# Kernel optimization log

Hardware: AMD Instinct MI355X
Metric: run time of the kernel (lower is better)

The kernel has to match this reference:

```python
import jax, jax.numpy as jnp
import numpy as np

B = 4096      # batch
F = 26        # sparse fields
V = 100000    # vocab per field
D = 64        # emb_dim
A = 64        # att_vector
ND = 13       # dense features
FEA = ND + D  # 77, BN / DNN input width
HID = [FEA, 256, 128, 64]
EPS = 1e-5


def setup_inputs() -> dict:
    key = jax.random.key(0)
    ks = jax.random.split(key, 20)
    s = 0.05  # matches .normal_(0, 0.05) init
    inp = {
        "sx": jax.random.randint(ks[0], (B, F), 0, V),
        "dx": jax.random.normal(ks[1], (B, ND), dtype=jnp.float32),
        "emb_table": jax.random.normal(ks[2], (F, V, D), dtype=jnp.float32) * s,
        "att_w_W": jax.random.normal(ks[3], (D, A), dtype=jnp.float32) * s,
        "att_w_b": jnp.zeros((A,), jnp.float32),
        "att_d_W": jax.random.normal(ks[4], (A, 1), dtype=jnp.float32) * s,
        "att_d_b": jnp.zeros((1,), jnp.float32),
        "bn_gamma": jnp.ones((FEA,), jnp.float32),
        "bn_beta": jnp.zeros((FEA,), jnp.float32),
        "w1": jax.random.normal(ks[5], (HID[0], HID[1]), dtype=jnp.float32) * s,
        "b1": jnp.zeros((HID[1],), jnp.float32),
        "w2": jax.random.normal(ks[6], (HID[1], HID[2]), dtype=jnp.float32) * s,
        "b2": jnp.zeros((HID[2],), jnp.float32),
        "w3": jax.random.normal(ks[7], (HID[2], HID[3]), dtype=jnp.float32) * s,
        "b3": jnp.zeros((HID[3],), jnp.float32),
        "wf": jax.random.normal(ks[8], (HID[3], 1), dtype=jnp.float32) * s,
        "bf": jnp.zeros((1,), jnp.float32),
    }
    return inp


def _afm_forward(sx, dx, emb_table, att_w_W, att_w_b, att_d_W, att_d_b,
                 bn_gamma, bn_beta, w1, b1, w2, b2, w3, b3, wf, bf):
    # embedding gather: [B, F, D]
    embeds = emb_table[jnp.arange(F)[None, :], sx]
    # all pairwise field interactions (upper-triangular pairs)
    i1, i2 = np.triu_indices(F, k=1)          # P = F*(F-1)/2 = 325
    bi = embeds[:, i1, :] * embeds[:, i2, :]  # [B, P, D]
    # attention MLP + softmax-weighted sum pooling over pairs
    a = jax.nn.relu(jnp.einsum("bpd,da->bpa", bi, att_w_W) + att_w_b)
    scores = jnp.einsum("bpa,ao->bpo", a, att_d_W) + att_d_b  # [B, P, 1]
    w = jax.nn.softmax(scores, axis=1)
    att_out = jnp.sum(w * bi, axis=1)         # [B, D]
    # concat with dense, batchnorm (training-mode batch stats, biased var)
    x = jnp.concatenate([att_out, dx], axis=-1)  # [B, FEA]
    mu = jnp.mean(x, axis=0)
    var = jnp.mean((x - mu) ** 2, axis=0)
    x = (x - mu) * jax.lax.rsqrt(var + EPS) * bn_gamma + bn_beta
    # DNN tower (dropout=0.0 -> identity) + final linear + sigmoid
    x = jax.nn.relu(x @ w1 + b1)
    x = jax.nn.relu(x @ w2 + b2)
    x = jax.nn.relu(x @ w3 + b3)
    out = jax.nn.sigmoid(x @ wf + bf)
    return jnp.squeeze(out, axis=-1)          # [B]


def reference(sx, dx, emb_table, att_w_W, att_w_b, att_d_W, att_d_b,
              bn_gamma, bn_beta, w1, b1, w2, b2, w3, b3, wf, bf):
    return _afm_forward(sx, dx, emb_table, att_w_W, att_w_b, att_d_W, att_d_b,
                        bn_gamma, bn_beta, w1, b1, w2, b2, w3, b3, wf, bf)
```

## Files before the change

kernel.cpp:

```cpp
#include <hip/hip_runtime.h>
#include <hip/hip_bf16.h>
#include <math.h>

#define BSZ   4096
#define F     26
#define VOC   100000
#define D     64
#define AD    64
#define ND    13
#define FEA   77
#define NPAIR 325
#define NPAD  336
#define MT    21
#define EP    68
#define H1    256
#define H2    128
#define H3    64
#define EPSF  1e-5f
#define MROW  4

typedef __attribute__((ext_vector_type(8))) short short8;
typedef __attribute__((ext_vector_type(4))) float f32x4;

union FragU { short8 s; unsigned int u[4]; };

__device__ __forceinline__ unsigned int pk2bf(float a, float b) {
  __hip_bfloat162 h = __float22bfloat162_rn(make_float2(a, b));
  return *reinterpret_cast<unsigned int*>(&h);
}
__device__ __forceinline__ unsigned short f2bf(float f) {
  unsigned int u = __float_as_uint(f);
  u += 0x7fffu + ((u >> 16) & 1u);
  return (unsigned short)(u >> 16);
}
template<int CTRL>
__device__ __forceinline__ float dpp_add(float x) {
  int xi = __builtin_bit_cast(int, x);
  int yi = __builtin_amdgcn_update_dpp(xi, xi, CTRL, 0xf, 0xf, false);
  return x + __builtin_bit_cast(float, yi);
}
__device__ __forceinline__ float row16_sum(float x) {
  x = dpp_add<0xB1>(x);
  x = dpp_add<0x4E>(x);
  x = dpp_add<0x124>(x);
  x = dpp_add<0x128>(x);
  return x;
}
__device__ __forceinline__ float bcast_lane(float v, int l) {
  return __builtin_bit_cast(float,
      __builtin_amdgcn_readlane(__builtin_bit_cast(int, v), l));
}

__global__ __launch_bounds__(256, 4) void k_attn(
    const int* __restrict__ sx, const float* __restrict__ dx,
    const float* __restrict__ emb, const float* __restrict__ attW,
    const float* __restrict__ attb, const float* __restrict__ attdW,
    const float* __restrict__ attdb, float* __restrict__ x,
    float* __restrict__ partS, float* __restrict__ partQ)
{
  __shared__ __align__(16) float e_all[4][27 * EP];
  __shared__ __align__(16) float sc_all[4][NPAD];
  __shared__ float xblk[4][80];
  __shared__ unsigned short pt[NPAD];

  const int t    = threadIdx.x;
  const int lane = t & 63;
  const int wv   = t >> 6;
  const int b    = __builtin_amdgcn_readfirstlane(blockIdx.x * 4 + wv);

  for (int p = t; p < NPAD; p += 256) {
    int f1 = 26, f2 = 26;
    if (p < NPAIR) {
      int i = 0, rem = p;
      while (rem >= F - 1 - i) { rem -= F - 1 - i; ++i; }
      f1 = i; f2 = i + 1 + rem;
    }
    pt[p] = (unsigned short)(f1 | (f2 << 8));
  }

  float* e_w  = e_all[wv];
  float* sc_w = sc_all[wv];

  {
    const int* sxb = sx + b * F;
    int rows[F];
    #pragma unroll
    for (int f = 0; f < F; ++f) rows[f] = sxb[f];
    float vf[F];
    #pragma unroll
    for (int f = 0; f < F; ++f)
      vf[f] = emb[((size_t)f * VOC + rows[f]) * D + lane];
    #pragma unroll
    for (int f = 0; f < F; ++f) e_w[f * EP + lane] = vf[f];
    e_w[26 * EP + lane] = 0.f;
  }

  short8 bfrag[2][4];
  float bj[4], dwj[4];
  {
    const int kb = (lane >> 4) * 8;
    const int cl = lane & 15;
    #pragma unroll
    for (int kk = 0; kk < 2; ++kk)
      #pragma unroll
      for (int n = 0; n < 4; ++n)
        #pragma unroll
        for (int j = 0; j < 8; ++j) {
          int k = kk * 32 + kb + j;
          bfrag[kk][n][j] = (short)f2bf(attW[k * AD + n * 16 + cl]);
        }
    #pragma unroll
    for (int n = 0; n < 4; ++n) {
      bj[n]  = attb[n * 16 + cl];
      dwj[n] = attdW[n * 16 + cl];
    }
  }
  const float db0 = attdb[0];

  __syncthreads();

  const int row16 = lane & 15;
  const int kgrp  = lane >> 4;
  const int k0    = kgrp * 8;
  const f32x4 zero4 = {0.f, 0.f, 0.f, 0.f};
  #pragma unroll 2
  for (int m = 0; m < MT; ++m) {
    const int prow = m * 16 + row16;
    const unsigned short pp = pt[prow];
    const float* r1 = &e_w[(pp & 0xff) * EP];
    const float* r2 = &e_w[(pp >> 8) * EP];
    f32x4 xv0 = *(const f32x4*)&r1[k0];
    f32x4 xv1 = *(const f32x4*)&r1[k0 + 4];
    f32x4 yv0 = *(const f32x4*)&r2[k0];
    f32x4 yv1 = *(const f32x4*)&r2[k0 + 4];
    f32x4 xv2 = *(const f32x4*)&r1[32 + k0];
    f32x4 xv3 = *(const f32x4*)&r1[32 + k0 + 4];
    f32x4 yv2 = *(const f32x4*)&r2[32 + k0];
    f32x4 yv3 = *(const f32x4*)&r2[32 + k0 + 4];
    f32x4 pa = xv0 * yv0;
    f32x4 pb = xv1 * yv1;
    f32x4 pc = xv2 * yv2;
    f32x4 pd = xv3 * yv3;
    FragU a0, a1;
    a0.u[0] = pk2bf(pa[0], pa[1]); a0.u[1] = pk2bf(pa[2], pa[3]);
    a0.u[2] = pk2bf(pb[0], pb[1]); a0.u[3] = pk2bf(pb[2], pb[3]);
    a1.u[0] = pk2bf(pc[0], pc[1]); a1.u[1] = pk2bf(pc[2], pc[3]);
    a1.u[2] = pk2bf(pd[0], pd[1]); a1.u[3] = pk2bf(pd[2], pd[3]);

    f32x4 acc[4];
    #pragma unroll
    for (int n = 0; n < 4; ++n) {
      acc[n] = __builtin_amdgcn_mfma_f32_16x16x32_bf16(a0.s, bfrag[0][n], zero4, 0, 0, 0);
      acc[n] = __builtin_amdgcn_mfma_f32_16x16x32_bf16(a1.s, bfrag[1][n], acc[n], 0, 0, 0);
    }
    f32x4 vale = zero4;
    #pragma unroll
    for (int n = 0; n < 4; ++n) {
      f32x4 rl = __builtin_elementwise_max(acc[n] + bj[n], zero4);
      vale = rl * dwj[n] + vale;
    }
    float s0 = row16_sum(vale[0]) + db0;
    float s1 = row16_sum(vale[1]) + db0;
    float s2 = row16_sum(vale[2]) + db0;
    float s3 = row16_sum(vale[3]) + db0;
    if (row16 == 0) {
      float4 o = {s0, s1, s2, s3};
      *(float4*)&sc_w[m * 16 + kgrp * 4] = o;
    }
  }

  float sv[6], ev[6];
  float mx = -1e30f;
  #pragma unroll
  for (int i = 0; i < 6; ++i) {
    int idx = lane + 64 * i;
    sv[i] = (idx < NPAIR) ? sc_w[idx] : -1e30f;
    mx = fmaxf(mx, sv[i]);
  }
  #pragma unroll
  for (int off = 32; off; off >>= 1) mx = fmaxf(mx, __shfl_xor(mx, off));
  float s = 0.f;
  #pragma unroll
  for (int i = 0; i < 6; ++i) {
    int idx = lane + 64 * i;
    ev[i] = (idx < NPAIR) ? __expf(sv[i] - mx) : 0.f;
    s += ev[i];
  }
  #pragma unroll
  for (int off = 32; off; off >>= 1) s += __shfl_xor(s, off);
  const float invZ = 1.f / s;

  float ef[F];
  #pragma unroll
  for (int f = 0; f < F; ++f) ef[f] = e_w[f * EP + lane];

  float pa0 = 0.f, pa1 = 0.f, pa2 = 0.f, pa3 = 0.f;
  {
    int p = 0;
    #pragma unroll
    for (int f1 = 0; f1 < F - 1; ++f1) {
      #pragma unroll
      for (int f2 = f1 + 1; f2 < F; ++f2) {
        const float w = bcast_lane(ev[p >> 6], p & 63);
        const float prod = ef[f1] * ef[f2];
        if ((p & 3) == 0)      pa0 = fmaf(w, prod, pa0);
        else if ((p & 3) == 1) pa1 = fmaf(w, prod, pa1);
        else if ((p & 3) == 2) pa2 = fmaf(w, prod, pa2);
        else                   pa3 = fmaf(w, prod, pa3);
        ++p;
      }
    }
  }
  const float att = ((pa0 + pa1) + (pa2 + pa3)) * invZ;

  x[(size_t)b * FEA + lane] = att;
  xblk[wv][lane] = att;
  if (lane < ND) {
    float dv = dx[b * ND + lane];
    x[(size_t)b * FEA + D + lane] = dv;
    xblk[wv][D + lane] = dv;
  }
  __syncthreads();

  if (t < FEA) {
    float x0 = xblk[0][t], x1 = xblk[1][t], x2 = xblk[2][t], x3 = xblk[3][t];
    float sS = (x0 + x1) + (x2 + x3);
    float sQ = (x0 * x0 + x1 * x1) + (x2 * x2 + x3 * x3);
    const int bkt = (blockIdx.x & 7) * 80 + t;
    atomicAdd(&partS[bkt], sS);
    atomicAdd(&partQ[bkt], sQ);
  }
}

__global__ __launch_bounds__(256) void k_mlp(
    const float* __restrict__ x,
    const float* __restrict__ partS, const float* __restrict__ partQ,
    const float* __restrict__ gamma, const float* __restrict__ beta,
    const float* __restrict__ w1, const float* __restrict__ b1,
    const float* __restrict__ w2, const float* __restrict__ b2,
    const float* __restrict__ w3, const float* __restrict__ b3,
    const float* __restrict__ wf, const float* __restrict__ bf,
    float* __restrict__ out)
{
  __shared__ float scs[80], shs[80];
  __shared__ float xn[MROW][80];
  __shared__ float h1s[MROW][H1];
  __shared__ float h2s[MROW][H2];
  __shared__ float h3s[MROW][H3];
  const int t = threadIdx.x;
  const int b0 = blockIdx.x * MROW;

  if (t < FEA) {
    float S = 0.f, Q = 0.f;
    #pragma unroll
    for (int k = 0; k < 8; ++k) {
      S += partS[k * 80 + t];
      Q += partQ[k * 80 + t];
    }
    float mu  = S * (1.f / BSZ);
    float var = Q * (1.f / BSZ) - mu * mu;
    float scl = gamma[t] * rsqrtf(var + EPSF);
    scs[t] = scl;
    shs[t] = beta[t] - mu * scl;
  }
  __syncthreads();

  for (int k = t; k < MROW * FEA; k += 256) {
    int r = k / FEA, f = k % FEA;
    xn[r][f] = x[(size_t)(b0 + r) * FEA + f] * scs[f] + shs[f];
  }
  __syncthreads();

  {
    float acc[MROW];
    const float bb = b1[t];
    #pragma unroll
    for (int r = 0; r < MROW; ++r) acc[r] = bb;
    for (int d0 = 0; d0 < FEA; d0 += 11) {
      float wl[11];
      #pragma unroll
      for (int u = 0; u < 11; ++u) wl[u] = w1[(d0 + u) * H1 + t];
      #pragma unroll
      for (int u = 0; u < 11; ++u)
        #pragma unroll
        for (int r = 0; r < MROW; ++r)
          acc[r] = fmaf(xn[r][d0 + u], wl[u], acc[r]);
    }
    #pragma unroll
    for (int r = 0; r < MROW; ++r) h1s[r][t] = fmaxf(acc[r], 0.f);
  }
  __syncthreads();

  {
    const int j = t & 127;
    const int rb = (t >> 7) * 2;
    float acc0 = b2[j], acc1 = acc0;
    for (int c0 = 0; c0 < H1; c0 += 16) {
      float wl[16];
      #pragma unroll
      for (int u = 0; u < 16; ++u) wl[u] = w2[(c0 + u) * H2 + j];
      #pragma unroll
      for (int u = 0; u < 16; ++u) {
        acc0 = fmaf(h1s[rb + 0][c0 + u], wl[u], acc0);
        acc1 = fmaf(h1s[rb + 1][c0 + u], wl[u], acc1);
      }
    }
    h2s[rb + 0][j] = fmaxf(acc0, 0.f);
    h2s[rb + 1][j] = fmaxf(acc1, 0.f);
  }
  __syncthreads();

  {
    const int j = t & 63;
    const int r = t >> 6;
    float acc = b3[j];
    for (int c0 = 0; c0 < H2; c0 += 16) {
      float wl[16];
      #pragma unroll
      for (int u = 0; u < 16; ++u) wl[u] = w3[(c0 + u) * H3 + j];
      #pragma unroll
      for (int u = 0; u < 16; ++u)
        acc = fmaf(h2s[r][c0 + u], wl[u], acc);
    }
    h3s[r][j] = fmaxf(acc, 0.f);
  }
  __syncthreads();

  if (t < MROW * 8) {
    const int r = t >> 3;
    const int g = t & 7;
    float acc = 0.f;
    #pragma unroll
    for (int u = 0; u < 8; ++u)
      acc = fmaf(h3s[r][g * 8 + u], wf[g * 8 + u], acc);
    acc = dpp_add<0xB1>(acc);
    acc = dpp_add<0x4E>(acc);
    acc = dpp_add<0x124>(acc);
    if (g == 0)
      out[b0 + r] = 1.f / (1.f + __expf(-(acc + bf[0])));
  }
}

extern "C" void kernel_launch(void* const* d_in, const int* in_sizes, int n_in,
                              void* d_out, int out_size, void* d_ws, size_t ws_size,
                              hipStream_t stream) {
  const int*   sx    = (const int*)  d_in[0];
  const float* dx    = (const float*)d_in[1];
  const float* emb   = (const float*)d_in[2];
  const float* attW  = (const float*)d_in[3];
  const float* attb  = (const float*)d_in[4];
  const float* attdW = (const float*)d_in[5];
  const float* attdb = (const float*)d_in[6];
  const float* gamma = (const float*)d_in[7];
  const float* beta  = (const float*)d_in[8];
  const float* w1    = (const float*)d_in[9];
  const float* b1    = (const float*)d_in[10];
  const float* w2    = (const float*)d_in[11];
  const float* b2    = (const float*)d_in[12];
  const float* w3    = (const float*)d_in[13];
  const float* b3    = (const float*)d_in[14];
  const float* wf    = (const float*)d_in[15];
  const float* bf    = (const float*)d_in[16];
  float* out = (float*)d_out;

  float* x     = (float*)d_ws;
  float* partS = x + (size_t)BSZ * FEA;
  float* partQ = partS + 8 * 80;

  hipMemsetAsync(partS, 0, 2 * 8 * 80 * sizeof(float), stream);
  k_attn<<<BSZ / 4, 256, 0, stream>>>(sx, dx, emb, attW, attb, attdW, attdb,
                                      x, partS, partQ);
  k_mlp<<<BSZ / 4, 256, 0, stream>>>(x, partS, partQ, gamma, beta,
                                     w1, b1, w2, b2, w3, b3, wf, bf, out);
}
```

Before: 65.29 us.

## Store gathered embeddings as bf16 in LDS with vectorized float4 gather

```diff
diff --git a/kernel.cpp b/kernel.cpp
--- a/kernel.cpp
+++ b/kernel.cpp
@@ -12,7 +12,7 @@
 #define NPAIR 325
 #define NPAD  336
 #define MT    21
-#define EP    68
+#define ERS   36
 #define H1    256
 #define H2    128
 #define H3    64
@@ -32,6 +32,12 @@
   unsigned int u = __float_as_uint(f);
   u += 0x7fffu + ((u >> 16) & 1u);
   return (unsigned short)(u >> 16);
+}
+__device__ __forceinline__ float bflo(unsigned int u) {
+  return __uint_as_float(u << 16);
+}
+__device__ __forceinline__ float bfhi(unsigned int u) {
+  return __uint_as_float(u & 0xffff0000u);
 }
 template<int CTRL>
 __device__ __forceinline__ float dpp_add(float x) {
@@ -51,14 +57,14 @@
       __builtin_amdgcn_readlane(__builtin_bit_cast(int, v), l));
 }
 
-__global__ __launch_bounds__(256, 4) void k_attn(
+__global__ __launch_bounds__(256, 6) void k_attn(
     const int* __restrict__ sx, const float* __restrict__ dx,
     const float* __restrict__ emb, const float* __restrict__ attW,
     const float* __restrict__ attb, const float* __restrict__ attdW,
     const float* __restrict__ attdb, float* __restrict__ x,
     float* __restrict__ partS, float* __restrict__ partQ)
 {
-  __shared__ __align__(16) float e_all[4][27 * EP];
+  __shared__ __align__(16) unsigned int e_all[4][27 * ERS];
   __shared__ __align__(16) float sc_all[4][NPAD];
   __shared__ float xblk[4][80];
   __shared__ unsigned short pt[NPAD];
@@ -78,21 +84,31 @@
     pt[p] = (unsigned short)(f1 | (f2 << 8));
   }
 
-  float* e_w  = e_all[wv];
+  unsigned int* e_w = e_all[wv];
   float* sc_w = sc_all[wv];
 
   {
-    const int* sxb = sx + b * F;
-    int rows[F];
-    #pragma unroll
-    for (int f = 0; f < F; ++f) rows[f] = sxb[f];
-    float vf[F];
-    #pragma unroll
-    for (int f = 0; f < F; ++f)
-      vf[f] = emb[((size_t)f * VOC + rows[f]) * D + lane];
-    #pragma unroll
-    for (int f = 0; f < F; ++f) e_w[f * EP + lane] = vf[f];
-    e_w[26 * EP + lane] = 0.f;
+    int rowsv[7]; float4 vv[7];
+    #pragma unroll
+    for (int i = 0; i < 7; ++i) {
+      int k = lane + 64 * i, f = k >> 4;
+      rowsv[i] = (f < F) ? sx[b * F + f] : 0;
+    }
+    #pragma unroll
+    for (int i = 0; i < 7; ++i) {
+      int k = lane + 64 * i, f = k >> 4, q = k & 15;
+      float4 v = {0.f, 0.f, 0.f, 0.f};
+      if (f < F) v = *(const float4*)&emb[((size_t)f * VOC + rowsv[i]) * D + q * 4];
+      vv[i] = v;
+    }
+    #pragma unroll
+    for (int i = 0; i < 7; ++i) {
+      int k = lane + 64 * i, f = k >> 4, q = k & 15;
+      if (f < 27) {
+        uint2 o = { pk2bf(vv[i].x, vv[i].y), pk2bf(vv[i].z, vv[i].w) };
+        *(uint2*)&e_w[f * ERS + 2 * q] = o;
+      }
+    }
   }
 
   short8 bfrag[2][4];
@@ -121,31 +137,26 @@
 
   const int row16 = lane & 15;
   const int kgrp  = lane >> 4;
-  const int k0    = kgrp * 8;
+  const int ku    = kgrp * 4;
   const f32x4 zero4 = {0.f, 0.f, 0.f, 0.f};
-  #pragma unroll 2
   for (int m = 0; m < MT; ++m) {
     const int prow = m * 16 + row16;
     const unsigned short pp = pt[prow];
-    const float* r1 = &e_w[(pp & 0xff) * EP];
-    const float* r2 = &e_w[(pp >> 8) * EP];
-    f32x4 xv0 = *(const f32x4*)&r1[k0];
-    f32x4 xv1 = *(const f32x4*)&r1[k0 + 4];
-    f32x4 yv0 = *(const f32x4*)&r2[k0];
-    f32x4 yv1 = *(const f32x4*)&r2[k0 + 4];
-    f32x4 xv2 = *(const f32x4*)&r1[32 + k0];
-    f32x4 xv3 = *(const f32x4*)&r1[32 + k0 + 4];
-    f32x4 yv2 = *(const f32x4*)&r2[32 + k0];
-    f32x4 yv3 = *(const f32x4*)&r2[32 + k0 + 4];
-    f32x4 pa = xv0 * yv0;
-    f32x4 pb = xv1 * yv1;
-    f32x4 pc = xv2 * yv2;
-    f32x4 pd = xv3 * yv3;
+    const unsigned int* r1 = &e_w[(pp & 0xff) * ERS];
+    const unsigned int* r2 = &e_w[(pp >> 8) * ERS];
+    uint4 u1a = *(const uint4*)&r1[ku];
+    uint4 u2a = *(const uint4*)&r2[ku];
+    uint4 u1b = *(const uint4*)&r1[16 + ku];
+    uint4 u2b = *(const uint4*)&r2[16 + ku];
     FragU a0, a1;
-    a0.u[0] = pk2bf(pa[0], pa[1]); a0.u[1] = pk2bf(pa[2], pa[3]);
-    a0.u[2] = pk2bf(pb[0], pb[1]); a0.u[3] = pk2bf(pb[2], pb[3]);
-    a1.u[0] = pk2bf(pc[0], pc[1]); a1.u[1] = pk2bf(pc[2], pc[3]);
-    a1.u[2] = pk2bf(pd[0], pd[1]); a1.u[3] = pk2bf(pd[2], pd[3]);
+    a0.u[0] = pk2bf(bflo(u1a.x)*bflo(u2a.x), bfhi(u1a.x)*bfhi(u2a.x));
+    a0.u[1] = pk2bf(bflo(u1a.y)*bflo(u2a.y), bfhi(u1a.y)*bfhi(u2a.y));
+    a0.u[2] = pk2bf(bflo(u1a.z)*bflo(u2a.z), bfhi(u1a.z)*bfhi(u2a.z));
+    a0.u[3] = pk2bf(bflo(u1a.w)*bflo(u2a.w), bfhi(u1a.w)*bfhi(u2a.w));
+    a1.u[0] = pk2bf(bflo(u1b.x)*bflo(u2b.x), bfhi(u1b.x)*bfhi(u2b.x));
+    a1.u[1] = pk2bf(bflo(u1b.y)*bflo(u2b.y), bfhi(u1b.y)*bfhi(u2b.y));
+    a1.u[2] = pk2bf(bflo(u1b.z)*bflo(u2b.z), bfhi(u1b.z)*bfhi(u2b.z));
+    a1.u[3] = pk2bf(bflo(u1b.w)*bflo(u2b.w), bfhi(u1b.w)*bfhi(u2b.w));
 
     f32x4 acc[4];
     #pragma unroll
@@ -190,9 +201,13 @@
   for (int off = 32; off; off >>= 1) s += __shfl_xor(s, off);
   const float invZ = 1.f / s;
 
+  const int shl = (lane & 1) ? 0 : 16;
   float ef[F];
   #pragma unroll
-  for (int f = 0; f < F; ++f) ef[f] = e_w[f * EP + lane];
+  for (int f = 0; f < F; ++f) {
+    unsigned int u = e_w[f * ERS + (lane >> 1)];
+    ef[f] = __uint_as_float((u << shl) & 0xffff0000u);
+  }
 
   float pa0 = 0.f, pa1 = 0.f, pa2 = 0.f, pa3 = 0.f;
   {
```

After: 74.31 us. +13.8%, slower.
